# Performance work log

Hardware: AMD Instinct MI355X
Metric: run time of the kernel (lower is better)

Reference implementation:

```python
import jax, jax.numpy as jnp
import numpy as np

B, CIN, H, W = 32, 256, 56, 56
COUT, KH, KW = 256, 3, 3
IN_RANK, OUT_RANK = 64, 64
STRIDE = (1, 1)
PADDING = ((1, 1), (1, 1))


def setup_inputs() -> dict:
    key = jax.random.key(0)
    k1, k2, k3, k4, k5 = jax.random.split(key, 5)
    # xavier-ish scales (not load-bearing for correctness, just realistic magnitudes)
    x = jax.random.normal(k1, (B, CIN, H, W), dtype=jnp.float32)
    first_factor = jax.random.normal(k2, (IN_RANK, CIN), dtype=jnp.float32) * (1.0 / np.sqrt(CIN))
    core_tensor = jax.random.normal(k3, (OUT_RANK, IN_RANK, KH, KW), dtype=jnp.float32) * (1.0 / np.sqrt(IN_RANK * KH * KW))
    last_factor = jax.random.normal(k4, (COUT, OUT_RANK), dtype=jnp.float32) * (1.0 / np.sqrt(OUT_RANK))
    bias = jax.random.normal(k5, (COUT,), dtype=jnp.float32) * 0.01
    return {"x": x, "first_factor": first_factor, "core_tensor": core_tensor,
            "last_factor": last_factor, "bias": bias}


def _recover_weight(core, last, first):
    # weight[o,c,h,w] = sum_{r,s} last[o,r] * core[r,s,h,w] * first[s,c]
    # (tucker_to_tensor with mode-0 factor last_factor and mode-1 factor first_factor.T)
    return jnp.einsum('or,rshw,sc->ochw', last, core, first)


def reference(x, first_factor, core_tensor, last_factor, bias):
    weight = _recover_weight(core_tensor, last_factor, first_factor)  # [COUT, CIN, KH, KW]
    out = jax.lax.conv_general_dilated(
        x, weight,
        window_strides=STRIDE,
        padding=PADDING,
        dimension_numbers=('NCHW', 'OIHW', 'NCHW'),
        feature_group_count=1,
    )
    return out + bias[None, :, None, None]
```

## Files before the change

kernel.cpp:

```cpp
#include <hip/hip_runtime.h>


typedef __attribute__((ext_vector_type(8))) short short8;
typedef __attribute__((ext_vector_type(4))) short short4v;
typedef __attribute__((ext_vector_type(4))) float f32x4;

#define B_    32
#define CIN_  256
#define H_    56
#define W_    56
#define HW_   (H_*W_)
#define COUT_ 256
#define HP_   58
#define WP_   64

#define OFF_FIRSTW  0u
#define OFF_COREW   32768u
#define OFF_LASTW   106496u
#define OFF_X1P     139264u

__device__ __forceinline__ unsigned short f2bf(float f) {
  union { float f; unsigned int u; } v; v.f = f;
  return (unsigned short)((v.u + 0x7FFFu + ((v.u >> 16) & 1u)) >> 16);
}
__device__ __forceinline__ short4v pack4(f32x4 a) {
  short4v p;
  p.x = (short)f2bf(a.x); p.y = (short)f2bf(a.y);
  p.z = (short)f2bf(a.z); p.w = (short)f2bf(a.w);
  return p;
}

__global__ __launch_bounds__(256) void prep_kernel(
    const float* __restrict__ first,
    const float* __restrict__ core,
    const float* __restrict__ last,
    unsigned short* __restrict__ ws16) {
  int i = blockIdx.x * 256 + threadIdx.x;
  if (i < 16384) {
    ws16[(OFF_FIRSTW >> 1) + i] = f2bf(first[i]);
  } else if (i < 53248) {
    int j = i - 16384;
    int t = j >> 12, r = (j >> 6) & 63, s = j & 63;
    ws16[(OFF_COREW >> 1) + j] = f2bf(core[(r * 64 + s) * 9 + t]);
  } else {
    ws16[(OFF_LASTW >> 1) + (i - 53248)] = f2bf(last[i - 53248]);
  }
}

__global__ __launch_bounds__(256, 6) void stageA_kernel(
    const float* __restrict__ x,
    unsigned short* __restrict__ ws16) {
  const unsigned short* firstW = ws16 + (OFF_FIRSTW >> 1);
  unsigned short* x1p = ws16 + (OFF_X1P >> 1);

  int tid = threadIdx.x, wave = tid >> 6, lane = tid & 63;
  int quad = lane >> 4, l15 = lane & 15;
  int bid0 = blockIdx.x;
  int bid = (bid0 & 7) * 232 + (bid0 >> 3);
  int b = bid / HP_, hp = bid - b * HP_;
  size_t rowbase = (size_t)(b * HP_ + hp) * (WP_ * 64);

  if (hp == 0 || hp == HP_ - 1) {
    short8 z = {0,0,0,0,0,0,0,0};
#pragma unroll
    for (int i = 0; i < 2; ++i)
      *(short8*)(x1p + rowbase + (size_t)(tid + i * 256) * 8) = z;
    return;
  }

  int h = hp - 1;
  int wp = wave * 16 + l15;
  bool valid = (wp >= 1 && wp <= 56);
  int wsrc = valid ? (wp - 1) : 0;
  const float* xcol = x + (size_t)b * (CIN_ * HW_) + h * W_ + wsrc;

  f32x4 acc[4] = {{0,0,0,0},{0,0,0,0},{0,0,0,0},{0,0,0,0}};
#pragma unroll 2
  for (int c0 = 0; c0 < CIN_; c0 += 32) {
    const float* p = xcol + (size_t)(c0 + quad * 8) * HW_;
    float xv[8];
#pragma unroll
    for (int j = 0; j < 8; ++j) xv[j] = p[(size_t)j * HW_];
    short8 bfrag;
#pragma unroll
    for (int j = 0; j < 8; ++j) bfrag[j] = (short)f2bf(xv[j]);
#pragma unroll
    for (int mt = 0; mt < 4; ++mt) {
      short8 af = *(const short8*)(firstW + (mt * 16 + l15) * CIN_ + c0 + quad * 8);
      acc[mt] = __builtin_amdgcn_mfma_f32_16x16x32_bf16(af, bfrag, acc[mt], 0, 0, 0);
    }
  }
  short4v zero4 = {0,0,0,0};
#pragma unroll
  for (int mt = 0; mt < 4; ++mt) {
    short4v r = valid ? pack4(acc[mt]) : zero4;
    *(short4v*)(x1p + rowbase + (size_t)wp * 64 + mt * 16 + quad * 4) = r;
  }
}

#define XTS 72
__global__ __launch_bounds__(256, 4) void fusedBC_kernel(
    const unsigned short* __restrict__ ws16,
    const float* __restrict__ bias,
    float* __restrict__ out) {
  __shared__ unsigned short yt[64 * XTS];
  const unsigned short* coreW = ws16 + (OFF_COREW >> 1);
  const unsigned short* lastW = ws16 + (OFF_LASTW >> 1);
  const unsigned short* x1p   = ws16 + (OFF_X1P >> 1);

  int tid = threadIdx.x, wave = tid >> 6, lane = tid & 63;
  int quad = lane >> 4, l15 = lane & 15;
  int bid0 = blockIdx.x;
  int bid = (bid0 & 7) * 224 + (bid0 >> 3);
  int b = bid / H_, h = bid - b * H_;
  int w = wave * 16 + l15;

  const unsigned short* xw = x1p + (size_t)(b * HP_ + h) * (WP_ * 64)
                             + (size_t)w * 64 + quad * 8;

  f32x4 acc[4] = {{0,0,0,0},{0,0,0,0},{0,0,0,0},{0,0,0,0}};
#pragma unroll
  for (int kh = 0; kh < 3; ++kh) {
#pragma unroll
    for (int kw = 0; kw < 3; ++kw) {
      int t = kh * 3 + kw;
#pragma unroll
      for (int k0 = 0; k0 < 64; k0 += 32) {
        short8 bfrag = *(const short8*)(xw + (size_t)(kh * WP_ + kw) * 64 + k0);
#pragma unroll
        for (int mt = 0; mt < 4; ++mt) {
          short8 af = *(const short8*)(coreW + (t * 64 + mt * 16 + l15) * 64 + k0 + quad * 8);
          acc[mt] = __builtin_amdgcn_mfma_f32_16x16x32_bf16(af, bfrag, acc[mt], 0, 0, 0);
        }
      }
    }
  }

#pragma unroll
  for (int mt = 0; mt < 4; ++mt)
    *(short4v*)&yt[w * XTS + mt * 16 + quad * 4] = pack4(acc[mt]);

  f32x4 acc2[16];
#pragma unroll
  for (int mt = 0; mt < 16; ++mt) acc2[mt] = (f32x4){0, 0, 0, 0};
#pragma unroll
  for (int k0 = 0; k0 < 64; k0 += 32) {
    short8 bfrag = *(const short8*)&yt[w * XTS + k0 + quad * 8];
#pragma unroll
    for (int mt = 0; mt < 16; ++mt) {
      short8 af = *(const short8*)(lastW + (mt * 16 + l15) * 64 + k0 + quad * 8);
      acc2[mt] = __builtin_amdgcn_mfma_f32_16x16x32_bf16(af, bfrag, acc2[mt], 0, 0, 0);
    }
  }

  if (w < W_) {
    float* ob = out + (size_t)b * (COUT_ * HW_) + h * W_ + w;
#pragma unroll
    for (int mt = 0; mt < 16; ++mt) {
      float4 bv = *(const float4*)(bias + mt * 16 + quad * 4);
      int o = mt * 16 + quad * 4;
      ob[(size_t)(o + 0) * HW_] = acc2[mt].x + bv.x;
      ob[(size_t)(o + 1) * HW_] = acc2[mt].y + bv.y;
      ob[(size_t)(o + 2) * HW_] = acc2[mt].z + bv.z;
      ob[(size_t)(o + 3) * HW_] = acc2[mt].w + bv.w;
    }
  }
}

extern "C" void kernel_launch(void* const* d_in, const int* in_sizes, int n_in,
                              void* d_out, int out_size, void* d_ws, size_t ws_size,
                              hipStream_t stream) {
  const float* x     = (const float*)d_in[0];
  const float* first = (const float*)d_in[1];
  const float* core  = (const float*)d_in[2];
  const float* last  = (const float*)d_in[3];
  const float* bias  = (const float*)d_in[4];
  float* out = (float*)d_out;
  unsigned short* ws16 = (unsigned short*)d_ws;

  prep_kernel<<<272, 256, 0, stream>>>(first, core, last, ws16);
  stageA_kernel<<<B_ * HP_, 256, 0, stream>>>(x, ws16);
  fusedBC_kernel<<<B_ * H_, 256, 0, stream>>>(ws16, bias, out);
}
```

Before: 310.8 us.

## Prefetch operands with double buffering and chunk final GEMM to cut registers

Stage A now double-buffers the x loads across channel chunks and stages its bf16 output through shared memory, so each wave writes contiguous 16-byte rows to global memory. The fused B/C kernel prefetches the next tap's activation fragments while issuing MFMAs for the current tap. It also splits the 256-output-channel GEMM into four groups of 64, storing each group as it finishes, so far fewer accumulators stay live and the occupancy hint rises from 4 to 5 blocks. The costs are more shared memory and a sync-free LDS round trip per wave in stage A, plus reloading the yt fragment once per output group.

```diff
diff --git a/kernel.cpp b/kernel.cpp
--- a/kernel.cpp
+++ b/kernel.cpp
@@ -47,9 +47,11 @@
   }
 }
 
+#define SATS 72
 __global__ __launch_bounds__(256, 6) void stageA_kernel(
     const float* __restrict__ x,
     unsigned short* __restrict__ ws16) {
+  __shared__ unsigned short st[4][16][SATS];
   const unsigned short* firstW = ws16 + (OFF_FIRSTW >> 1);
   unsigned short* x1p = ws16 + (OFF_X1P >> 1);
 
@@ -75,31 +77,45 @@
   const float* xcol = x + (size_t)b * (CIN_ * HW_) + h * W_ + wsrc;
 
   f32x4 acc[4] = {{0,0,0,0},{0,0,0,0},{0,0,0,0},{0,0,0,0}};
-#pragma unroll 2
-  for (int c0 = 0; c0 < CIN_; c0 += 32) {
-    const float* p = xcol + (size_t)(c0 + quad * 8) * HW_;
-    float xv[8];
-#pragma unroll
-    for (int j = 0; j < 8; ++j) xv[j] = p[(size_t)j * HW_];
+  float xv[2][8];
+#pragma unroll
+  for (int j = 0; j < 8; ++j) xv[0][j] = xcol[(size_t)(quad * 8 + j) * HW_];
+
+#pragma unroll
+  for (int cc = 0; cc < 8; ++cc) {
+    int cur = cc & 1;
+    if (cc < 7) {
+      const float* p = xcol + (size_t)((cc + 1) * 32 + quad * 8) * HW_;
+#pragma unroll
+      for (int j = 0; j < 8; ++j) xv[cur ^ 1][j] = p[(size_t)j * HW_];
+    }
     short8 bfrag;
 #pragma unroll
-    for (int j = 0; j < 8; ++j) bfrag[j] = (short)f2bf(xv[j]);
+    for (int j = 0; j < 8; ++j) bfrag[j] = (short)f2bf(xv[cur][j]);
 #pragma unroll
     for (int mt = 0; mt < 4; ++mt) {
-      short8 af = *(const short8*)(firstW + (mt * 16 + l15) * CIN_ + c0 + quad * 8);
+      short8 af = *(const short8*)(firstW + (mt * 16 + l15) * CIN_ + cc * 32 + quad * 8);
       acc[mt] = __builtin_amdgcn_mfma_f32_16x16x32_bf16(af, bfrag, acc[mt], 0, 0, 0);
     }
   }
+
   short4v zero4 = {0,0,0,0};
 #pragma unroll
   for (int mt = 0; mt < 4; ++mt) {
     short4v r = valid ? pack4(acc[mt]) : zero4;
-    *(short4v*)(x1p + rowbase + (size_t)wp * 64 + mt * 16 + quad * 4) = r;
+    *(short4v*)&st[wave][l15][mt * 16 + quad * 4] = r;
+  }
+#pragma unroll
+  for (int i = 0; i < 2; ++i) {
+    int idx = i * 512 + lane * 8;
+    int r = idx >> 6, s0 = idx & 63;
+    short8 v = *(const short8*)&st[wave][r][s0];
+    *(short8*)(x1p + rowbase + (size_t)wave * 1024 + idx) = v;
   }
 }
 
 #define XTS 72
-__global__ __launch_bounds__(256, 4) void fusedBC_kernel(
+__global__ __launch_bounds__(256, 5) void fusedBC_kernel(
     const unsigned short* __restrict__ ws16,
     const float* __restrict__ bias,
     float* __restrict__ out) {
@@ -119,50 +135,57 @@
                              + (size_t)w * 64 + quad * 8;
 
   f32x4 acc[4] = {{0,0,0,0},{0,0,0,0},{0,0,0,0},{0,0,0,0}};
-#pragma unroll
-  for (int kh = 0; kh < 3; ++kh) {
-#pragma unroll
-    for (int kw = 0; kw < 3; ++kw) {
-      int t = kh * 3 + kw;
-#pragma unroll
-      for (int k0 = 0; k0 < 64; k0 += 32) {
-        short8 bfrag = *(const short8*)(xw + (size_t)(kh * WP_ + kw) * 64 + k0);
-#pragma unroll
-        for (int mt = 0; mt < 4; ++mt) {
-          short8 af = *(const short8*)(coreW + (t * 64 + mt * 16 + l15) * 64 + k0 + quad * 8);
-          acc[mt] = __builtin_amdgcn_mfma_f32_16x16x32_bf16(af, bfrag, acc[mt], 0, 0, 0);
-        }
-      }
-    }
+  short8 bc0 = *(const short8*)(xw);
+  short8 bc1 = *(const short8*)(xw + 32);
+#pragma unroll
+  for (int t = 0; t < 9; ++t) {
+    short8 bn0, bn1;
+    if (t < 8) {
+      int kh2 = (t + 1) / 3, kw2 = (t + 1) - kh2 * 3;
+      const unsigned short* p = xw + (size_t)(kh2 * WP_ + kw2) * 64;
+      bn0 = *(const short8*)p;
+      bn1 = *(const short8*)(p + 32);
+    }
+#pragma unroll
+    for (int mt = 0; mt < 4; ++mt) {
+      short8 af = *(const short8*)(coreW + (t * 64 + mt * 16 + l15) * 64 + quad * 8);
+      acc[mt] = __builtin_amdgcn_mfma_f32_16x16x32_bf16(af, bc0, acc[mt], 0, 0, 0);
+    }
+#pragma unroll
+    for (int mt = 0; mt < 4; ++mt) {
+      short8 af = *(const short8*)(coreW + (t * 64 + mt * 16 + l15) * 64 + 32 + quad * 8);
+      acc[mt] = __builtin_amdgcn_mfma_f32_16x16x32_bf16(af, bc1, acc[mt], 0, 0, 0);
+    }
+    if (t < 8) { bc0 = bn0; bc1 = bn1; }
   }
 
 #pragma unroll
   for (int mt = 0; mt < 4; ++mt)
     *(short4v*)&yt[w * XTS + mt * 16 + quad * 4] = pack4(acc[mt]);
 
-  f32x4 acc2[16];
-#pragma unroll
-  for (int mt = 0; mt < 16; ++mt) acc2[mt] = (f32x4){0, 0, 0, 0};
-#pragma unroll
-  for (int k0 = 0; k0 < 64; k0 += 32) {
-    short8 bfrag = *(const short8*)&yt[w * XTS + k0 + quad * 8];
-#pragma unroll
-    for (int mt = 0; mt < 16; ++mt) {
-      short8 af = *(const short8*)(lastW + (mt * 16 + l15) * 64 + k0 + quad * 8);
-      acc2[mt] = __builtin_amdgcn_mfma_f32_16x16x32_bf16(af, bfrag, acc2[mt], 0, 0, 0);
-    }
-  }
-
-  if (w < W_) {
-    float* ob = out + (size_t)b * (COUT_ * HW_) + h * W_ + w;
-#pragma unroll
-    for (int mt = 0; mt < 16; ++mt) {
-      float4 bv = *(const float4*)(bias + mt * 16 + quad * 4);
-      int o = mt * 16 + quad * 4;
-      ob[(size_t)(o + 0) * HW_] = acc2[mt].x + bv.x;
-      ob[(size_t)(o + 1) * HW_] = acc2[mt].y + bv.y;
-      ob[(size_t)(o + 2) * HW_] = acc2[mt].z + bv.z;
-      ob[(size_t)(o + 3) * HW_] = acc2[mt].w + bv.w;
+  float* ob = out + (size_t)b * (COUT_ * HW_) + h * W_ + w;
+#pragma unroll
+  for (int g = 0; g < 4; ++g) {
+    f32x4 a2[4] = {{0,0,0,0},{0,0,0,0},{0,0,0,0},{0,0,0,0}};
+#pragma unroll
+    for (int k0 = 0; k0 < 64; k0 += 32) {
+      short8 bfrag = *(const short8*)&yt[w * XTS + k0 + quad * 8];
+#pragma unroll
+      for (int m = 0; m < 4; ++m) {
+        short8 af = *(const short8*)(lastW + (g * 64 + m * 16 + l15) * 64 + k0 + quad * 8);
+        a2[m] = __builtin_amdgcn_mfma_f32_16x16x32_bf16(af, bfrag, a2[m], 0, 0, 0);
+      }
+    }
+    if (w < W_) {
+#pragma unroll
+      for (int m = 0; m < 4; ++m) {
+        int o = g * 64 + m * 16 + quad * 4;
+        float4 bv = *(const float4*)(bias + o);
+        ob[(size_t)(o + 0) * HW_] = a2[m].x + bv.x;
+        ob[(size_t)(o + 1) * HW_] = a2[m].y + bv.y;
+        ob[(size_t)(o + 2) * HW_] = a2[m].z + bv.z;
+        ob[(size_t)(o + 3) * HW_] = a2[m].w + bv.w;
+      }
     }
   }
 }
```

Result: faster. 303.5 us (-2.4%).
